# Optimization experiments

Measured on AMD Instinct MI355X. Metric: run time of the kernel, lower is better.

Reference implementation:

```python
import jax, jax.numpy as jnp
import numpy as np

MARGIN = 1.0
TEMPERATURE = 1.0
EPS = 1e-12  # matches torch F.normalize eps default scale behavior (eps=1e-12)


def _l2_normalize(x):
    # torch F.normalize: x / max(||x||, eps)
    norm = jnp.sqrt(jnp.sum(x * x, axis=-1, keepdims=True))
    return x / jnp.maximum(norm, EPS)


def setup_inputs() -> dict:
    key = jax.random.key(0)
    k1, k2 = jax.random.split(key)
    N, D = 8192, 1024
    image_embeds = jax.random.normal(k1, (N, D), dtype=jnp.float32)
    text_embeds = jax.random.normal(k2, (N, D), dtype=jnp.float32)
    return {"image_embeds": image_embeds, "text_embeds": text_embeds}


def reference(image_embeds, text_embeds):
    # L2 normalize; cosine similarity of unit vectors == dot product (GEMM)
    img = _l2_normalize(image_embeds)   # [N, D]
    txt = _l2_normalize(text_embeds)    # [N, D]
    sim = jnp.einsum('nd,md->nm', img, txt) / TEMPERATURE  # [N, N]
    positives = jnp.diagonal(sim)                          # [N]
    # logsumexp over rows of (sim - margin); margin shifts all entries uniformly
    lse = jax.nn.logsumexp(sim - MARGIN, axis=-1)          # [N]
    return jnp.mean(lse - positives)
```

## Files before the change

### kernel.cpp

```cpp
#include <hip/hip_runtime.h>
#include <hip/hip_bf16.h>
#include <stdint.h>

#define N_ROWS 8192
#define DIM    1024
#define BM 128
#define BN 128
#define BKF 128
#define NT (DIM / BKF)
#define TILES_PB 8
#define VSTEPS (NT * TILES_PB)

typedef float   f32x4  __attribute__((ext_vector_type(4)));
typedef int     i32x4  __attribute__((ext_vector_type(4)));
typedef int     i32x8  __attribute__((ext_vector_type(8)));

__device__ __forceinline__ float row_sum16(float x) {
    x += __int_as_float(__builtin_amdgcn_update_dpp(
            0, __float_as_int(x), 0x128 , 0xf, 0xf, true));
    x += __int_as_float(__builtin_amdgcn_update_dpp(
            0, __float_as_int(x), 0x124 , 0xf, 0xf, true));
    x += __int_as_float(__builtin_amdgcn_update_dpp(
            0, __float_as_int(x), 0x122 , 0xf, 0xf, true));
    x += __int_as_float(__builtin_amdgcn_update_dpp(
            0, __float_as_int(x), 0x121 , 0xf, 0xf, true));
    return x;
}

__global__ __launch_bounds__(256) void nrm_kernel(
    const float* __restrict__ img, const float* __restrict__ txt,
    uint8_t* __restrict__ img_f8, uint8_t* __restrict__ txt_f8,
    float* __restrict__ diag, float* __restrict__ S)
{
    const int t    = threadIdx.x;
    const int lane = t & 63;
    const int w    = t >> 6;
    __shared__ float red[3][4];

#pragma unroll 1
    for (int r = 0; r < 8; ++r) {
        const int row = blockIdx.x * 8 + r;

        const float4 a = ((const float4*)(img + (size_t)row * DIM))[t];
        const float4 b = ((const float4*)(txt + (size_t)row * DIM))[t];

        float sa = a.x * a.x + a.y * a.y + a.z * a.z + a.w * a.w;
        float sb = b.x * b.x + b.y * b.y + b.z * b.z + b.w * b.w;
#pragma unroll
        for (int d = 1; d < 64; d <<= 1) {
            sa += __shfl_xor(sa, d, 64);
            sb += __shfl_xor(sb, d, 64);
        }
        if (lane == 0) { red[0][w] = sa; red[1][w] = sb; }
        __syncthreads();
        sa = red[0][0] + red[0][1] + red[0][2] + red[0][3];
        sb = red[1][0] + red[1][1] + red[1][2] + red[1][3];

        const float ia = 1.0f / fmaxf(sqrtf(sa), 1e-12f);
        const float ib = 1.0f / fmaxf(sqrtf(sb), 1e-12f);

        int ra = 0, rb = 0;
        ra = __builtin_amdgcn_cvt_pk_fp8_f32(a.x * ia, a.y * ia, ra, false);
        ra = __builtin_amdgcn_cvt_pk_fp8_f32(a.z * ia, a.w * ia, ra, true);
        rb = __builtin_amdgcn_cvt_pk_fp8_f32(b.x * ib, b.y * ib, rb, false);
        rb = __builtin_amdgcn_cvt_pk_fp8_f32(b.z * ib, b.w * ib, rb, true);
        ((int*)(img_f8 + (size_t)row * DIM))[t] = ra;
        ((int*)(txt_f8 + (size_t)row * DIM))[t] = rb;

        float dp = (a.x * b.x + a.y * b.y + a.z * b.z + a.w * b.w) * ia * ib;
#pragma unroll
        for (int d = 1; d < 64; d <<= 1) dp += __shfl_xor(dp, d, 64);
        if (lane == 0) red[2][w] = dp;
        __syncthreads();
        if (t == 0) {
            diag[row] = red[2][0] + red[2][1] + red[2][2] + red[2][3];
            S[row] = 0.0f;
        }
    }
}

__global__ __launch_bounds__(256) void sim_lse_kernel(
    const uint8_t* __restrict__ A, const uint8_t* __restrict__ B,
    float* __restrict__ S)
{
    __shared__ __align__(16) uint8_t smem[2 * 2 * BM * BKF];

    const int t     = threadIdx.x;
    const int lane  = t & 63;
    const int w     = t >> 6;
    const int waveM = w >> 1;
    const int waveN = w & 1;
    const int lr    = lane & 15;
    const int q     = lane >> 4;
    const int swz   = lr & 7;

    const int rowA0 = blockIdx.y * BM;
    const uint8_t* Ablk = A + (size_t)rowA0 * DIM;
    const uint8_t* Bgrp = B + (size_t)blockIdx.x * TILES_PB * BN * DIM;

    const uint32_t lo_off = (uint32_t)(((2 * q) ^ swz) * 16);

    const uint8_t* pA[4];
    const uint8_t* pB[4];
    uint32_t ldsA[4], ldsB[4];
#pragma unroll
    for (int is = 0; is < 4; ++is) {
        const int c   = is * 256 + t;
        const int row = c >> 3;
        const int col = (c & 7) ^ (row & 7);
        pA[is] = Ablk + (size_t)row * DIM + col * 16;
        pB[is] = Bgrp + (size_t)row * DIM + col * 16;
        ldsA[is] = (uint32_t)c * 16;
        ldsB[is] = 16384u + (uint32_t)c * 16;
    }

    auto stage_inc = [&](uint32_t ldsbase) {
#pragma unroll
        for (int is = 0; is < 4; ++is) {
            __builtin_amdgcn_global_load_lds(
                (const __attribute__((address_space(1))) void*)pA[is],
                (__attribute__((address_space(3))) void*)&smem[ldsbase + ldsA[is]],
                16, 0, 0);
            __builtin_amdgcn_global_load_lds(
                (const __attribute__((address_space(1))) void*)pB[is],
                (__attribute__((address_space(3))) void*)&smem[ldsbase + ldsB[is]],
                16, 0, 0);
        }
    };

    uint32_t adrA  = (uint32_t)((waveM * 64 + lr) * BKF) + lo_off;
    uint32_t adrAh = (uint32_t)((waveM * 64 + lr) * BKF) + (lo_off ^ 16u);
    uint32_t adrB  = 16384u + (uint32_t)((waveN * 64 + lr) * BKF) + lo_off;
    uint32_t adrBh = 16384u + (uint32_t)((waveN * 64 + lr) * BKF) + (lo_off ^ 16u);

    f32x4 acc[4][4] = {};

    stage_inc(0u);
#pragma unroll
    for (int is = 0; is < 4; ++is) { pA[is] += 128; pB[is] += 128; }
    asm volatile("s_waitcnt vmcnt(0)" ::: "memory");
    __builtin_amdgcn_s_barrier();

    const float L2E = 1.44269504088896f;
    const int rowbase = rowA0 + waveM * 64;

#pragma unroll 1
    for (int v = 0; v < VSTEPS; ++v) {
        const uint32_t nxt = (uint32_t)(((v & 1) ^ 1) << 15);

        if (v < VSTEPS - 1) {
            stage_inc(nxt);
            const bool wrap = ((v + 1) & (NT - 1)) == (NT - 1);
            const int dA = wrap ? -(BKF * (NT - 1)) : BKF;
            const int dB = wrap ? (BN * DIM - BKF * (NT - 1)) : BKF;
#pragma unroll
            for (int is = 0; is < 4; ++is) { pA[is] += dA; pB[is] += dB; }
        }

        i32x8 af[4], bfr[4];
#pragma unroll
        for (int mi = 0; mi < 4; ++mi) {
            i32x4 lo = *(const i32x4*)&smem[adrA  + mi * 2048];
            i32x4 hi = *(const i32x4*)&smem[adrAh + mi * 2048];
            af[mi] = __builtin_shufflevector(lo, hi, 0, 1, 2, 3, 4, 5, 6, 7);
        }
#pragma unroll
        for (int ni = 0; ni < 4; ++ni) {
            i32x4 lo = *(const i32x4*)&smem[adrB  + ni * 2048];
            i32x4 hi = *(const i32x4*)&smem[adrBh + ni * 2048];
            bfr[ni] = __builtin_shufflevector(lo, hi, 0, 1, 2, 3, 4, 5, 6, 7);
        }
#pragma unroll
        for (int mi = 0; mi < 4; ++mi)
#pragma unroll
            for (int ni = 0; ni < 4; ++ni)
                acc[mi][ni] = __builtin_amdgcn_mfma_scale_f32_16x16x128_f8f6f4(
                    af[mi], bfr[ni], acc[mi][ni],
                    0 , 0 ,
                    0, 127 , 0, 127 );

        adrA ^= 32768u; adrAh ^= 32768u; adrB ^= 32768u; adrBh ^= 32768u;

        if ((v & (NT - 1)) == NT - 1) {
#pragma unroll
            for (int mi = 0; mi < 4; ++mi) {
                float p0 = 0.f, p1 = 0.f, p2 = 0.f, p3 = 0.f;
#pragma unroll
                for (int ni = 0; ni < 4; ++ni) {
                    p0 += exp2f(acc[mi][ni].x * L2E - L2E);
                    p1 += exp2f(acc[mi][ni].y * L2E - L2E);
                    p2 += exp2f(acc[mi][ni].z * L2E - L2E);
                    p3 += exp2f(acc[mi][ni].w * L2E - L2E);
                    acc[mi][ni] = (f32x4){0.f, 0.f, 0.f, 0.f};
                }
                p0 = row_sum16(p0); p1 = row_sum16(p1);
                p2 = row_sum16(p2); p3 = row_sum16(p3);
                if ((lane & 15) == 0) {
                    float* dst = &S[rowbase + mi * 16 + (lane >> 4) * 4];
                    atomicAdd(dst + 0, p0); atomicAdd(dst + 1, p1);
                    atomicAdd(dst + 2, p2); atomicAdd(dst + 3, p3);
                }
            }
        }

        asm volatile("s_waitcnt vmcnt(0)" ::: "memory");
        __builtin_amdgcn_s_barrier();
    }
}

__global__ __launch_bounds__(1024) void fin_kernel(
    const float* __restrict__ S, const float* __restrict__ diag,
    float* __restrict__ out)
{
    const int t = threadIdx.x;
    float s = 0.f;
    for (int i = t; i < N_ROWS; i += 1024) s += logf(S[i]) - diag[i];
#pragma unroll
    for (int d = 1; d < 64; d <<= 1) s += __shfl_xor(s, d, 64);
    __shared__ float red[16];
    if ((t & 63) == 0) red[t >> 6] = s;
    __syncthreads();
    if (t == 0) {
        float tot = 0.f;
#pragma unroll
        for (int i = 0; i < 16; ++i) tot += red[i];
        out[0] = tot * (1.0f / N_ROWS);
    }
}

extern "C" void kernel_launch(void* const* d_in, const int* in_sizes, int n_in,
                              void* d_out, int out_size, void* d_ws, size_t ws_size,
                              hipStream_t stream)
{
    const float* img = (const float*)d_in[0];
    const float* txt = (const float*)d_in[1];
    float* out = (float*)d_out;

    char* ws = (char*)d_ws;
    uint8_t* img_f8 = (uint8_t*)ws;
    uint8_t* txt_f8 = (uint8_t*)(ws + (size_t)N_ROWS * DIM);
    float*   S      = (float*)(ws + (size_t)N_ROWS * DIM * 2);
    float*   diag   = S + N_ROWS;

    nrm_kernel<<<N_ROWS / 8, 256, 0, stream>>>(img, txt, img_f8, txt_f8, diag, S);
    dim3 grid(N_ROWS / BN / TILES_PB, N_ROWS / BM);
    sim_lse_kernel<<<grid, 256, 0, stream>>>(img_f8, txt_f8, S);
    fin_kernel<<<1, 1024, 0, stream>>>(S, diag, out);
}
```

Baseline: 193.9 us.

## Fuse final reduction into GEMM via last-block counter, one row per wave in normalize

The normalize kernel now gives each wave a whole row, so the block-level LDS reductions and barriers go away, and the diagonal dot product is computed in the same pass as the norms. The final logsumexp/mean kernel is dropped. Instead, the last sim block to finish, detected with an atomic counter that the normalize kernel resets, does the reduction, which saves one launch. The grid axes are also swapped, so A row tiles map to blockIdx.x, which changes block scheduling order and L2 reuse. In exchange, every GEMM block pays for a threadfence and a global atomic at its end.

```diff
diff --git a/kernel.cpp b/kernel.cpp
--- a/kernel.cpp
+++ b/kernel.cpp
@@ -10,6 +10,7 @@
 #define NT (DIM / BKF)
 #define TILES_PB 8
 #define VSTEPS (NT * TILES_PB)
+#define NBLK (N_ROWS / BM * N_ROWS / BN / TILES_PB)
 
 typedef float   f32x4  __attribute__((ext_vector_type(4)));
 typedef int     i32x4  __attribute__((ext_vector_type(4)));
@@ -30,60 +31,62 @@
 __global__ __launch_bounds__(256) void nrm_kernel(
     const float* __restrict__ img, const float* __restrict__ txt,
     uint8_t* __restrict__ img_f8, uint8_t* __restrict__ txt_f8,
-    float* __restrict__ diag, float* __restrict__ S)
+    float* __restrict__ diag, float* __restrict__ S, int* __restrict__ cnt)
 {
     const int t    = threadIdx.x;
     const int lane = t & 63;
-    const int w    = t >> 6;
-    __shared__ float red[3][4];
-
-#pragma unroll 1
-    for (int r = 0; r < 8; ++r) {
-        const int row = blockIdx.x * 8 + r;
-
-        const float4 a = ((const float4*)(img + (size_t)row * DIM))[t];
-        const float4 b = ((const float4*)(txt + (size_t)row * DIM))[t];
-
-        float sa = a.x * a.x + a.y * a.y + a.z * a.z + a.w * a.w;
-        float sb = b.x * b.x + b.y * b.y + b.z * b.z + b.w * b.w;
-#pragma unroll
-        for (int d = 1; d < 64; d <<= 1) {
-            sa += __shfl_xor(sa, d, 64);
-            sb += __shfl_xor(sb, d, 64);
-        }
-        if (lane == 0) { red[0][w] = sa; red[1][w] = sb; }
-        __syncthreads();
-        sa = red[0][0] + red[0][1] + red[0][2] + red[0][3];
-        sb = red[1][0] + red[1][1] + red[1][2] + red[1][3];
-
-        const float ia = 1.0f / fmaxf(sqrtf(sa), 1e-12f);
-        const float ib = 1.0f / fmaxf(sqrtf(sb), 1e-12f);
-
+    const int wv   = t >> 6;
+    const int row  = blockIdx.x * 4 + wv;
+
+    const float4* ip = (const float4*)(img + (size_t)row * DIM);
+    const float4* tp = (const float4*)(txt + (size_t)row * DIM);
+
+    float4 a[4], b[4];
+    float sa = 0.f, sb = 0.f, dp = 0.f;
+#pragma unroll
+    for (int j = 0; j < 4; ++j) {
+        a[j] = ip[lane + 64 * j];
+        b[j] = tp[lane + 64 * j];
+        sa += a[j].x * a[j].x + a[j].y * a[j].y + a[j].z * a[j].z + a[j].w * a[j].w;
+        sb += b[j].x * b[j].x + b[j].y * b[j].y + b[j].z * b[j].z + b[j].w * b[j].w;
+        dp += a[j].x * b[j].x + a[j].y * b[j].y + a[j].z * b[j].z + a[j].w * b[j].w;
+    }
+#pragma unroll
+    for (int d = 1; d < 64; d <<= 1) {
+        sa += __shfl_xor(sa, d, 64);
+        sb += __shfl_xor(sb, d, 64);
+        dp += __shfl_xor(dp, d, 64);
+    }
+
+    const float ia = 1.0f / fmaxf(sqrtf(sa), 1e-12f);
+    const float ib = 1.0f / fmaxf(sqrtf(sb), 1e-12f);
+
+#pragma unroll
+    for (int j = 0; j < 4; ++j) {
         int ra = 0, rb = 0;
-        ra = __builtin_amdgcn_cvt_pk_fp8_f32(a.x * ia, a.y * ia, ra, false);
-        ra = __builtin_amdgcn_cvt_pk_fp8_f32(a.z * ia, a.w * ia, ra, true);
-        rb = __builtin_amdgcn_cvt_pk_fp8_f32(b.x * ib, b.y * ib, rb, false);
-        rb = __builtin_amdgcn_cvt_pk_fp8_f32(b.z * ib, b.w * ib, rb, true);
-        ((int*)(img_f8 + (size_t)row * DIM))[t] = ra;
-        ((int*)(txt_f8 + (size_t)row * DIM))[t] = rb;
-
-        float dp = (a.x * b.x + a.y * b.y + a.z * b.z + a.w * b.w) * ia * ib;
-#pragma unroll
-        for (int d = 1; d < 64; d <<= 1) dp += __shfl_xor(dp, d, 64);
-        if (lane == 0) red[2][w] = dp;
-        __syncthreads();
-        if (t == 0) {
-            diag[row] = red[2][0] + red[2][1] + red[2][2] + red[2][3];
-            S[row] = 0.0f;
-        }
+        ra = __builtin_amdgcn_cvt_pk_fp8_f32(a[j].x * ia, a[j].y * ia, ra, false);
+        ra = __builtin_amdgcn_cvt_pk_fp8_f32(a[j].z * ia, a[j].w * ia, ra, true);
+        rb = __builtin_amdgcn_cvt_pk_fp8_f32(b[j].x * ib, b[j].y * ib, rb, false);
+        rb = __builtin_amdgcn_cvt_pk_fp8_f32(b[j].z * ib, b[j].w * ib, rb, true);
+        ((int*)(img_f8 + (size_t)row * DIM))[lane + 64 * j] = ra;
+        ((int*)(txt_f8 + (size_t)row * DIM))[lane + 64 * j] = rb;
+    }
+
+    if (lane == 0) {
+        diag[row] = dp * ia * ib;
+        S[row] = 0.0f;
+        if (row == 0) *cnt = 0;
     }
 }
 
 __global__ __launch_bounds__(256) void sim_lse_kernel(
     const uint8_t* __restrict__ A, const uint8_t* __restrict__ B,
-    float* __restrict__ S)
+    float* __restrict__ S, const float* __restrict__ diag,
+    float* __restrict__ out, int* __restrict__ cnt)
 {
     __shared__ __align__(16) uint8_t smem[2 * 2 * BM * BKF];
+    __shared__ int lastblk;
+    __shared__ float fred[4];
 
     const int t     = threadIdx.x;
     const int lane  = t & 63;
@@ -94,9 +97,9 @@
     const int q     = lane >> 4;
     const int swz   = lr & 7;
 
-    const int rowA0 = blockIdx.y * BM;
+    const int rowA0 = blockIdx.x * BM;
     const uint8_t* Ablk = A + (size_t)rowA0 * DIM;
-    const uint8_t* Bgrp = B + (size_t)blockIdx.x * TILES_PB * BN * DIM;
+    const uint8_t* Bgrp = B + (size_t)blockIdx.y * TILES_PB * BN * DIM;
 
     const uint32_t lo_off = (uint32_t)(((2 * q) ^ swz) * 16);
 
@@ -206,25 +209,24 @@
         asm volatile("s_waitcnt vmcnt(0)" ::: "memory");
         __builtin_amdgcn_s_barrier();
     }
-}
-
-__global__ __launch_bounds__(1024) void fin_kernel(
-    const float* __restrict__ S, const float* __restrict__ diag,
-    float* __restrict__ out)
-{
-    const int t = threadIdx.x;
-    float s = 0.f;
-    for (int i = t; i < N_ROWS; i += 1024) s += logf(S[i]) - diag[i];
-#pragma unroll
-    for (int d = 1; d < 64; d <<= 1) s += __shfl_xor(s, d, 64);
-    __shared__ float red[16];
-    if ((t & 63) == 0) red[t >> 6] = s;
+
+    __threadfence();
     __syncthreads();
-    if (t == 0) {
-        float tot = 0.f;
-#pragma unroll
-        for (int i = 0; i < 16; ++i) tot += red[i];
-        out[0] = tot * (1.0f / N_ROWS);
+    if (t == 0) lastblk = (atomicAdd(cnt, 1) == NBLK - 1);
+    __syncthreads();
+    if (lastblk) {
+        float s = 0.f;
+        for (int i = t; i < N_ROWS; i += 256) {
+            const float sv = __hip_atomic_load(&S[i], __ATOMIC_RELAXED,
+                                               __HIP_MEMORY_SCOPE_AGENT);
+            s += logf(sv) - diag[i];
+        }
+#pragma unroll
+        for (int d = 1; d < 64; d <<= 1) s += __shfl_xor(s, d, 64);
+        if ((t & 63) == 0) fred[t >> 6] = s;
+        __syncthreads();
+        if (t == 0)
+            out[0] = (fred[0] + fred[1] + fred[2] + fred[3]) * (1.0f / N_ROWS);
     }
 }
 
@@ -241,9 +243,10 @@
     uint8_t* txt_f8 = (uint8_t*)(ws + (size_t)N_ROWS * DIM);
     float*   S      = (float*)(ws + (size_t)N_ROWS * DIM * 2);
     float*   diag   = S + N_ROWS;
-
-    nrm_kernel<<<N_ROWS / 8, 256, 0, stream>>>(img, txt, img_f8, txt_f8, diag, S);
-    dim3 grid(N_ROWS / BN / TILES_PB, N_ROWS / BM);
-    sim_lse_kernel<<<grid, 256, 0, stream>>>(img_f8, txt_f8, S);
-    fin_kernel<<<1, 1024, 0, stream>>>(S, diag, out);
-}
+    int*     cnt    = (int*)(diag + N_ROWS);
+
+    nrm_kernel<<<N_ROWS / 4, 256, 0, stream>>>(img, txt, img_f8, txt_f8,
+                                               diag, S, cnt);
+    dim3 grid(N_ROWS / BM, N_ROWS / BN / TILES_PB);
+    sim_lse_kernel<<<grid, 256, 0, stream>>>(img_f8, txt_f8, S, diag, out, cnt);
+}
```

Result: slower. 234.1 us (+20.8%).
